# Kernel optimization log

Measured on AMD Instinct MI355X. Metric: run time of the kernel, lower is better.

Reference implementation:

```python
import math
import jax, jax.numpy as jnp
import numpy as np

NUM_HEADS = 16

def _alibi_slopes(n):
    def pow2(n):
        start = 2 ** (-2 ** (-(math.log2(n) - 3)))
        return [start * start ** i for i in range(n)]
    if math.log2(n).is_integer():
        return pow2(n)
    c = 2 ** math.floor(math.log2(n))
    return pow2(c) + _alibi_slopes(2 * c)[0::2][: n - c]

def _alibi_bias(num_heads, L):
    pos = np.arange(L)
    rel = (pos[None, :] - pos[:, None]).astype(np.float32)  # [L, L]
    slopes = np.asarray(_alibi_slopes(num_heads), dtype=np.float32)[:, None, None]
    bias = slopes * rel[None, :, :]  # [H, L, L]
    causal = pos[None, :] <= pos[:, None]
    bias = np.where(causal[None, :, :], bias, -np.inf).astype(np.float32)
    return jnp.asarray(bias)[None]  # [1, H, L, L]

def setup_inputs() -> dict:
    key = jax.random.key(0)
    ks = jax.random.split(key, 4)
    B, L, D = 2, 2048, 1024
    x = jax.random.normal(ks[0], (B, L, D), dtype=jnp.float32)
    W_in = jax.random.normal(ks[1], (D, 3 * D), dtype=jnp.float32) * 0.02
    b_in = jnp.zeros((3 * D,), dtype=jnp.float32)
    W_out = jax.random.normal(ks[2], (D, D), dtype=jnp.float32) * 0.02
    b_out = jnp.zeros((D,), dtype=jnp.float32)
    return {"x": x, "W_in": W_in, "b_in": b_in, "W_out": W_out, "b_out": b_out}

def reference(x, W_in, b_in, W_out, b_out):
    B, L, D = x.shape
    H = NUM_HEADS
    Dh = D // H
    qkv = x @ W_in + b_in  # [B, L, 3D]
    q, k, v = jnp.split(qkv, 3, axis=-1)
    # [B, H, L, Dh]
    q = q.reshape(B, L, H, Dh).transpose(0, 2, 1, 3)
    k = k.reshape(B, L, H, Dh).transpose(0, 2, 1, 3)
    v = v.reshape(B, L, H, Dh).transpose(0, 2, 1, 3)
    attn = jnp.einsum("bhqd,bhkd->bhqk", q, k) * (1.0 / math.sqrt(Dh))
    attn = attn + _alibi_bias(H, L)  # ALiBi + causal mask (-inf above diag)
    p = jax.nn.softmax(attn, axis=-1)
    out = jnp.einsum("bhqk,bhkd->bhqd", p, v)
    out = out.transpose(0, 2, 1, 3).reshape(B, L, D)
    out = out @ W_out + b_out
    return out, k, v
```

## Files before the change

### kernel.cpp

```cpp
#include <hip/hip_runtime.h>
#include <math.h>

typedef __bf16 bf16x8 __attribute__((ext_vector_type(8)));
typedef float  f32x4  __attribute__((ext_vector_type(4)));
typedef unsigned short u16x4 __attribute__((ext_vector_type(4)));

#define BATCH  2
#define SEQ    2048
#define DMODEL 1024
#define NHEAD  16
#define DHEAD  64
#define MROWS  4096
#define N_QKV  3072
#define KDIM   1024
#define OUTSECT (MROWS*DMODEL)

__device__ inline __bf16 f2bf(float f) {
    unsigned u = __builtin_bit_cast(unsigned, f);
    unsigned r = (u + 0x7fffu + ((u >> 16) & 1u)) >> 16;
    return __builtin_bit_cast(__bf16, (unsigned short)r);
}

__device__ inline void gload16(const void* g, void* l) {
    __builtin_amdgcn_global_load_lds(
        (const __attribute__((address_space(1))) void*)g,
        (__attribute__((address_space(3))) void*)l, 16, 0, 0);
}


__global__ __launch_bounds__(256) void cvt_x_k(const float* __restrict__ x,
                                               __bf16* __restrict__ xb) {
    size_t i = (size_t)blockIdx.x * 256 + threadIdx.x;
    const float4* p = (const float4*)x + i * 2;
    float4 a = p[0], b = p[1];
    __bf16 o[8] = {f2bf(a.x), f2bf(a.y), f2bf(a.z), f2bf(a.w),
                   f2bf(b.x), f2bf(b.y), f2bf(b.z), f2bf(b.w)};
    *(bf16x8*)(xb + i * 8) = *(bf16x8*)o;
}

__global__ __launch_bounds__(256) void cvt_wt_k(const float* __restrict__ W,
                                                __bf16* __restrict__ Wt, int Nw) {
    __shared__ float t[64][65];
    const int k0 = blockIdx.y * 64, n0 = blockIdx.x * 64;
    const int tid = threadIdx.x;
    #pragma unroll
    for (int u = 0; u < 4; ++u) {
        int idx = u * 256 + tid;
        int r = idx >> 4, c4 = (idx & 15) << 2;
        float4 v = *(const float4*)&W[(size_t)(k0 + r) * Nw + n0 + c4];
        t[r][c4] = v.x; t[r][c4 + 1] = v.y; t[r][c4 + 2] = v.z; t[r][c4 + 3] = v.w;
    }
    __syncthreads();
    #pragma unroll
    for (int u = 0; u < 2; ++u) {
        int idx = u * 256 + tid;
        int n = idx >> 3, k8 = (idx & 7) << 3;
        __bf16 o[8];
        #pragma unroll
        for (int i = 0; i < 8; ++i) o[i] = f2bf(t[k8 + i][n]);
        *(bf16x8*)&Wt[(size_t)(n0 + n) * KDIM + k0 + k8] = *(bf16x8*)o;
    }
}

template<int MODE, int FI, int FJ>
__global__ __launch_bounds__(256) void gemm_bf(
    const __bf16* __restrict__ A, const __bf16* __restrict__ Bt,
    const float* __restrict__ bias,
    float* __restrict__ fo, float* __restrict__ kf, float* __restrict__ vf,
    __bf16* __restrict__ qb, __bf16* __restrict__ kb, __bf16* __restrict__ vb,
    int nbx)
{
    constexpr int BMt = FI * 32, BNt = FJ * 32;
    __shared__ __align__(16) __bf16 As[BMt * 64];
    __shared__ __align__(16) __bf16 Bs[BNt * 64];

    const int tid = threadIdx.x, wid = tid >> 6, lane = tid & 63;
    const int l16 = lane & 15, lq = lane >> 4;
    const int wm = wid >> 1, wn = wid & 1;

    const int nwg = gridDim.x;
    const int bid = blockIdx.x;
    const int swz = (bid & 7) * (nwg >> 3) + (bid >> 3);
    const int m0 = (swz / nbx) * BMt;
    const int n0 = (swz % nbx) * BNt;

    const int lr8 = lane >> 3;
    const int colE = ((lane & 7) ^ lr8) << 3;

    f32x4 acc[FI][FJ];
    #pragma unroll
    for (int i = 0; i < FI; ++i)
        #pragma unroll
        for (int j = 0; j < FJ; ++j)
            acc[i][j] = f32x4{0.f, 0.f, 0.f, 0.f};

    for (int k0 = 0; k0 < KDIM; k0 += 64) {
        __syncthreads();
        #pragma unroll
        for (int c = wid; c < FI * 4 + FJ * 4; c += 4) {
            const bool isA = (c < FI * 4);
            const int ch = isA ? c : c - FI * 4;
            const int row = ch * 8 + lr8;
            const __bf16* src = isA ? (A  + (size_t)(m0 + row) * KDIM + k0 + colE)
                                    : (Bt + (size_t)(n0 + row) * KDIM + k0 + colE);
            gload16(src, (isA ? As : Bs) + ch * 512);
        }
        __syncthreads();
        #pragma unroll
        for (int kk = 0; kk < 2; ++kk) {
            bf16x8 af[FI], bfg[FJ];
            #pragma unroll
            for (int i = 0; i < FI; ++i) {
                int r = wm * (FI * 16) + i * 16 + l16;
                af[i] = *(const bf16x8*)&As[r * 64 + ((kk * 32 + lq * 8) ^ ((r & 7) << 3))];
            }
            #pragma unroll
            for (int j = 0; j < FJ; ++j) {
                int r = wn * (FJ * 16) + j * 16 + l16;
                bfg[j] = *(const bf16x8*)&Bs[r * 64 + ((kk * 32 + lq * 8) ^ ((r & 7) << 3))];
            }
            #pragma unroll
            for (int i = 0; i < FI; ++i)
                #pragma unroll
                for (int j = 0; j < FJ; ++j)
                    acc[i][j] = __builtin_amdgcn_mfma_f32_16x16x32_bf16(af[i], bfg[j], acc[i][j], 0, 0, 0);
        }
    }

    #pragma unroll
    for (int i = 0; i < FI; ++i) {
        #pragma unroll
        for (int j = 0; j < FJ; ++j) {
            const int col  = n0 + wn * (FJ * 16) + j * 16 + l16;
            const int rowb = m0 + wm * (FI * 16) + i * 16 + lq * 4;
            float v[4];
            #pragma unroll
            for (int r = 0; r < 4; ++r) v[r] = acc[i][j][r] + bias[col];
            if (MODE == 1) {
                #pragma unroll
                for (int r = 0; r < 4; ++r)
                    fo[(size_t)(rowb + r) * DMODEL + col] = v[r];
            } else {
                const int which = col >> 10, rem = col & 1023;
                const int h = rem >> 6, dh = rem & 63;
                const int bb = rowb >> 11, ll = rowb & 2047;
                const size_t lidx = ((size_t)(bb * NHEAD + h) * SEQ + ll) * DHEAD + dh;
                if (which == 0) {
                    #pragma unroll
                    for (int r = 0; r < 4; ++r) qb[lidx + (size_t)r * DHEAD] = f2bf(v[r]);
                } else if (which == 1) {
                    #pragma unroll
                    for (int r = 0; r < 4; ++r) {
                        kf[lidx + (size_t)r * DHEAD] = v[r];
                        kb[lidx + (size_t)r * DHEAD] = f2bf(v[r]);
                    }
                } else {
                    u16x4 pk;
                    #pragma unroll
                    for (int r = 0; r < 4; ++r) {
                        vf[lidx + (size_t)r * DHEAD] = v[r];
                        pk[r] = __builtin_bit_cast(unsigned short, f2bf(v[r]));
                    }
                    *(u16x4*)&vb[((size_t)(bb * NHEAD + h) * DHEAD + dh) * SEQ + ll] = pk;
                }
            }
        }
    }
}

__global__ __launch_bounds__(256) void attn_k(
    const __bf16* __restrict__ Qb, const __bf16* __restrict__ Kb,
    const __bf16* __restrict__ Vb, __bf16* __restrict__ Ob)
{
    __shared__ __align__(16) __bf16 Qs[64 * 64];
    __shared__ __align__(16) __bf16 Ks[2][64 * 64];
    __shared__ __align__(16) __bf16 Vs[2][64 * 64];
    __shared__ __align__(16) __bf16 Ps[4 * 16 * 64];

    const int tid = threadIdx.x, wid = tid >> 6, lane = tid & 63;
    const int l16 = lane & 15, lq = lane >> 4;

    const int bid = blockIdx.x;
    const int t   = bid >> 3;
    const int qt  = 31 - (t >> 2);
    const int bh  = (bid & 7) * 4 + (t & 3);
    const int h = bh & 15, bb = bh >> 4;
    const int q0 = qt * 64;
    const size_t kvbase = (size_t)bh * SEQ * DHEAD;
    const float slope = exp2f(-0.5f * (float)(h + 1));
    const int qr0 = wid * 16;
    const int lr8 = lane >> 3;
    const int colE = ((lane & 7) ^ lr8) << 3;

    #pragma unroll
    for (int u = 0; u < 2; ++u) {
        int ch = u * 4 + wid;
        int row = ch * 8 + lr8;
        gload16(Qb + kvbase + (size_t)(q0 + row) * DHEAD + colE, Qs + ch * 512);
    }
    #pragma unroll
    for (int u = 0; u < 2; ++u) {
        int ch = u * 4 + wid;
        int row = ch * 8 + lr8;
        gload16(Kb + kvbase + (size_t)row * DHEAD + colE, Ks[0] + ch * 512);
        gload16(Vb + kvbase + (size_t)row * SEQ  + colE, Vs[0] + ch * 512);
    }
    __syncthreads();

    float mrow[4], lrow[4];
    f32x4 accO[4];
    #pragma unroll
    for (int r = 0; r < 4; ++r) { mrow[r] = -1e30f; lrow[r] = 0.f; }
    #pragma unroll
    for (int j = 0; j < 4; ++j) accO[j] = f32x4{0.f, 0.f, 0.f, 0.f};

    int cur = 0;
    for (int jt = 0; jt <= qt; ++jt) {
        const int j0 = jt * 64;

        if (jt < qt) {
            const int jn = j0 + 64;
            #pragma unroll
            for (int u = 0; u < 2; ++u) {
                int ch = u * 4 + wid;
                int row = ch * 8 + lr8;
                gload16(Kb + kvbase + (size_t)(jn + row) * DHEAD + colE, Ks[cur ^ 1] + ch * 512);
                gload16(Vb + kvbase + (size_t)row * SEQ + jn + colE,     Vs[cur ^ 1] + ch * 512);
            }
        }

        f32x4 s[4];
        #pragma unroll
        for (int nf = 0; nf < 4; ++nf) s[nf] = f32x4{0.f, 0.f, 0.f, 0.f};
        const int qrow = qr0 + l16;
        bf16x8 aq0 = *(const bf16x8*)&Qs[qrow * 64 + ((lq * 8) ^ ((qrow & 7) << 3))];
        bf16x8 aq1 = *(const bf16x8*)&Qs[qrow * 64 + ((32 + lq * 8) ^ ((qrow & 7) << 3))];
        __builtin_amdgcn_s_setprio(1);
        #pragma unroll
        for (int nf = 0; nf < 4; ++nf) {
            int kr = nf * 16 + l16;
            bf16x8 bk0 = *(const bf16x8*)&Ks[cur][kr * 64 + ((lq * 8) ^ ((kr & 7) << 3))];
            bf16x8 bk1 = *(const bf16x8*)&Ks[cur][kr * 64 + ((32 + lq * 8) ^ ((kr & 7) << 3))];
            s[nf] = __builtin_amdgcn_mfma_f32_16x16x32_bf16(aq0, bk0, s[nf], 0, 0, 0);
            s[nf] = __builtin_amdgcn_mfma_f32_16x16x32_bf16(aq1, bk1, s[nf], 0, 0, 0);
        }
        __builtin_amdgcn_s_setprio(0);

        #pragma unroll
        for (int r = 0; r < 4; ++r) {
            const int qi = q0 + qr0 + lq * 4 + r;
            float rm = -1e30f;
            #pragma unroll
            for (int nf = 0; nf < 4; ++nf) {
                int ki = j0 + nf * 16 + l16;
                float sc = s[nf][r] * 0.125f;
                sc = (ki <= qi) ? (sc + slope * (float)(ki - qi)) : -1e30f;
                s[nf][r] = sc;
                rm = fmaxf(rm, sc);
            }
            #pragma unroll
            for (int msk = 1; msk < 16; msk <<= 1)
                rm = fmaxf(rm, __shfl_xor(rm, msk));
            float mnew = fmaxf(mrow[r], rm);
            float rsum = 0.f;
            const int prow = lq * 4 + r;
            #pragma unroll
            for (int nf = 0; nf < 4; ++nf) {
                float p = __expf(s[nf][r] - mnew);
                Ps[wid * 1024 + prow * 64 + ((nf * 16 + l16) ^ ((prow & 7) << 3))] = f2bf(p);
                rsum += p;
            }
            #pragma unroll
            for (int msk = 1; msk < 16; msk <<= 1)
                rsum += __shfl_xor(rsum, msk);
            float scale = __expf(mrow[r] - mnew);
            lrow[r] = lrow[r] * scale + rsum;
            mrow[r] = mnew;
            #pragma unroll
            for (int nf = 0; nf < 4; ++nf) accO[nf][r] *= scale;
        }

        bf16x8 ap0 = *(const bf16x8*)&Ps[wid * 1024 + l16 * 64 + ((lq * 8) ^ ((l16 & 7) << 3))];
        bf16x8 ap1 = *(const bf16x8*)&Ps[wid * 1024 + l16 * 64 + ((32 + lq * 8) ^ ((l16 & 7) << 3))];
        __builtin_amdgcn_s_setprio(1);
        #pragma unroll
        for (int nf = 0; nf < 4; ++nf) {
            int vr = nf * 16 + l16;
            bf16x8 bv0 = *(const bf16x8*)&Vs[cur][vr * 64 + ((lq * 8) ^ ((vr & 7) << 3))];
            bf16x8 bv1 = *(const bf16x8*)&Vs[cur][vr * 64 + ((32 + lq * 8) ^ ((vr & 7) << 3))];
            accO[nf] = __builtin_amdgcn_mfma_f32_16x16x32_bf16(ap0, bv0, accO[nf], 0, 0, 0);
            accO[nf] = __builtin_amdgcn_mfma_f32_16x16x32_bf16(ap1, bv1, accO[nf], 0, 0, 0);
        }
        __builtin_amdgcn_s_setprio(0);

        __syncthreads();
        cur ^= 1;
    }

    #pragma unroll
    for (int nf = 0; nf < 4; ++nf) {
        #pragma unroll
        for (int r = 0; r < 4; ++r) {
            int qi = q0 + qr0 + lq * 4 + r;
            int dh = nf * 16 + l16;
            Ob[(size_t)(bb * SEQ + qi) * DMODEL + h * DHEAD + dh] = f2bf(accO[nf][r] / lrow[r]);
        }
    }
}

extern "C" void kernel_launch(void* const* d_in, const int* in_sizes, int n_in,
                              void* d_out, int out_size, void* d_ws, size_t ws_size,
                              hipStream_t stream) {
    const float* x     = (const float*)d_in[0];
    const float* W_in  = (const float*)d_in[1];
    const float* b_in  = (const float*)d_in[2];
    const float* W_out = (const float*)d_in[3];
    const float* b_out = (const float*)d_in[4];

    float* out = (float*)d_out;
    float* kf  = out + (size_t)OUTSECT;
    float* vf  = out + 2 * (size_t)OUTSECT;

    __bf16* qb = (__bf16*)d_out;
    __bf16* xb = (__bf16*)d_out + (size_t)OUTSECT;

    __bf16* ob  = (__bf16*)d_ws;
    __bf16* kb  = ob + (size_t)OUTSECT;
    __bf16* vb  = kb + (size_t)OUTSECT;
    __bf16* wti = vb + (size_t)OUTSECT;
    __bf16* wto = wti + (size_t)N_QKV * KDIM;

    cvt_x_k <<<2048, 256, 0, stream>>>(x, xb);
    cvt_wt_k<<<dim3(48, 16), 256, 0, stream>>>(W_in,  wti, N_QKV);
    cvt_wt_k<<<dim3(16, 16), 256, 0, stream>>>(W_out, wto, DMODEL);

    gemm_bf<0, 4, 4><<<768, 256, 0, stream>>>(xb, wti, b_in,
        nullptr, kf, vf, qb, kb, vb, N_QKV / 128);

    attn_k<<<1024, 256, 0, stream>>>(qb, kb, vb, ob);

    gemm_bf<1, 2, 4><<<512, 256, 0, stream>>>(ob, wto, b_out,
        out, nullptr, nullptr, nullptr, nullptr, nullptr, DMODEL / 128);
}
```

Measured before the change: 222.6 us.

## Fold softmax scale into Q, seed scores with ALiBi bias, use DPP reductions

Q is pre-scaled by 1/sqrt(d)*log2e in the QKV GEMM epilogue, so the attention loop uses exp2 directly. Score accumulators are initialised with an incrementally updated ALiBi bias, and the causal mask applies only on the diagonal tile, which removes per-element scaling, bias and compare work. Row max and sum reductions use DPP instead of shuffles, and the final normalisation multiplies by a reciprocal. The trade-off is that bias accumulation through repeated float adds may drift slightly, and the changes to bf16 rounding and bias ordering alter numerics a little.

```diff
diff --git a/kernel.cpp b/kernel.cpp
--- a/kernel.cpp
+++ b/kernel.cpp
@@ -15,6 +15,9 @@
 #define KDIM   1024
 #define OUTSECT (MROWS*DMODEL)
 
+#define LOG2E 1.44269504088896f
+#define QSCALE (0.125f * LOG2E)
+
 __device__ inline __bf16 f2bf(float f) {
     unsigned u = __builtin_bit_cast(unsigned, f);
     unsigned r = (u + 0x7fffu + ((u >> 16) & 1u)) >> 16;
@@ -25,6 +28,39 @@
     __builtin_amdgcn_global_load_lds(
         (const __attribute__((address_space(1))) void*)g,
         (__attribute__((address_space(3))) void*)l, 16, 0, 0);
+}
+
+__device__ inline float dpp_max16(float x) {
+    int v, t;
+    v = __builtin_bit_cast(int, x);
+    t = __builtin_amdgcn_update_dpp(v, v, 0xB1, 0xF, 0xF, false);
+    x = fmaxf(x, __builtin_bit_cast(float, t));
+    v = __builtin_bit_cast(int, x);
+    t = __builtin_amdgcn_update_dpp(v, v, 0x4E, 0xF, 0xF, false);
+    x = fmaxf(x, __builtin_bit_cast(float, t));
+    v = __builtin_bit_cast(int, x);
+    t = __builtin_amdgcn_update_dpp(v, v, 0x128, 0xF, 0xF, false);
+    x = fmaxf(x, __builtin_bit_cast(float, t));
+    v = __builtin_bit_cast(int, x);
+    t = __builtin_amdgcn_update_dpp(v, v, 0x140, 0xF, 0xF, false);
+    x = fmaxf(x, __builtin_bit_cast(float, t));
+    return x;
+}
+__device__ inline float dpp_sum16(float x) {
+    int v, t;
+    v = __builtin_bit_cast(int, x);
+    t = __builtin_amdgcn_update_dpp(v, v, 0xB1, 0xF, 0xF, false);
+    x += __builtin_bit_cast(float, t);
+    v = __builtin_bit_cast(int, x);
+    t = __builtin_amdgcn_update_dpp(v, v, 0x4E, 0xF, 0xF, false);
+    x += __builtin_bit_cast(float, t);
+    v = __builtin_bit_cast(int, x);
+    t = __builtin_amdgcn_update_dpp(v, v, 0x128, 0xF, 0xF, false);
+    x += __builtin_bit_cast(float, t);
+    v = __builtin_bit_cast(int, x);
+    t = __builtin_amdgcn_update_dpp(v, v, 0x140, 0xF, 0xF, false);
+    x += __builtin_bit_cast(float, t);
+    return x;
 }
 
 
@@ -147,7 +183,8 @@
                 const size_t lidx = ((size_t)(bb * NHEAD + h) * SEQ + ll) * DHEAD + dh;
                 if (which == 0) {
                     #pragma unroll
-                    for (int r = 0; r < 4; ++r) qb[lidx + (size_t)r * DHEAD] = f2bf(v[r]);
+                    for (int r = 0; r < 4; ++r)
+                        qb[lidx + (size_t)r * DHEAD] = f2bf(v[r] * QSCALE);
                 } else if (which == 1) {
                     #pragma unroll
                     for (int r = 0; r < 4; ++r) {
@@ -187,7 +224,7 @@
     const int h = bh & 15, bb = bh >> 4;
     const int q0 = qt * 64;
     const size_t kvbase = (size_t)bh * SEQ * DHEAD;
-    const float slope = exp2f(-0.5f * (float)(h + 1));
+    const float slope2 = exp2f(-0.5f * (float)(h + 1)) * LOG2E;
     const int qr0 = wid * 16;
     const int lr8 = lane >> 3;
     const int colE = ((lane & 7) ^ lr8) << 3;
@@ -207,6 +244,16 @@
     }
     __syncthreads();
 
+    float ct[4][4];
+    #pragma unroll
+    for (int r = 0; r < 4; ++r) {
+        const int qi = q0 + qr0 + lq * 4 + r;
+        #pragma unroll
+        for (int nf = 0; nf < 4; ++nf)
+            ct[r][nf] = slope2 * (float)(nf * 16 + l16 - qi);
+    }
+    const float dtj = slope2 * 64.f;
+
     float mrow[4], lrow[4];
     f32x4 accO[4];
     #pragma unroll
@@ -216,10 +263,8 @@
 
     int cur = 0;
     for (int jt = 0; jt <= qt; ++jt) {
-        const int j0 = jt * 64;
-
         if (jt < qt) {
-            const int jn = j0 + 64;
+            const int jn = (jt + 1) * 64;
             #pragma unroll
             for (int u = 0; u < 2; ++u) {
                 int ch = u * 4 + wid;
@@ -231,7 +276,18 @@
 
         f32x4 s[4];
         #pragma unroll
-        for (int nf = 0; nf < 4; ++nf) s[nf] = f32x4{0.f, 0.f, 0.f, 0.f};
+        for (int nf = 0; nf < 4; ++nf) {
+            #pragma unroll
+            for (int r = 0; r < 4; ++r) s[nf][r] = ct[r][nf];
+        }
+        if (jt == qt) {
+            #pragma unroll
+            for (int nf = 0; nf < 4; ++nf)
+                #pragma unroll
+                for (int r = 0; r < 4; ++r)
+                    if (nf * 16 + l16 > qr0 + lq * 4 + r) s[nf][r] = -3e38f;
+        }
+
         const int qrow = qr0 + l16;
         bf16x8 aq0 = *(const bf16x8*)&Qs[qrow * 64 + ((lq * 8) ^ ((qrow & 7) << 3))];
         bf16x8 aq1 = *(const bf16x8*)&Qs[qrow * 64 + ((32 + lq * 8) ^ ((qrow & 7) << 3))];
@@ -248,37 +304,31 @@
 
         #pragma unroll
         for (int r = 0; r < 4; ++r) {
-            const int qi = q0 + qr0 + lq * 4 + r;
-            float rm = -1e30f;
-            #pragma unroll
-            for (int nf = 0; nf < 4; ++nf) {
-                int ki = j0 + nf * 16 + l16;
-                float sc = s[nf][r] * 0.125f;
-                sc = (ki <= qi) ? (sc + slope * (float)(ki - qi)) : -1e30f;
-                s[nf][r] = sc;
-                rm = fmaxf(rm, sc);
-            }
-            #pragma unroll
-            for (int msk = 1; msk < 16; msk <<= 1)
-                rm = fmaxf(rm, __shfl_xor(rm, msk));
+            float rm = fmaxf(fmaxf(s[0][r], s[1][r]), fmaxf(s[2][r], s[3][r]));
+            rm = dpp_max16(rm);
             float mnew = fmaxf(mrow[r], rm);
-            float rsum = 0.f;
+            float p0 = __builtin_amdgcn_exp2f(s[0][r] - mnew);
+            float p1 = __builtin_amdgcn_exp2f(s[1][r] - mnew);
+            float p2 = __builtin_amdgcn_exp2f(s[2][r] - mnew);
+            float p3 = __builtin_amdgcn_exp2f(s[3][r] - mnew);
             const int prow = lq * 4 + r;
-            #pragma unroll
-            for (int nf = 0; nf < 4; ++nf) {
-                float p = __expf(s[nf][r] - mnew);
-                Ps[wid * 1024 + prow * 64 + ((nf * 16 + l16) ^ ((prow & 7) << 3))] = f2bf(p);
-                rsum += p;
-            }
-            #pragma unroll
-            for (int msk = 1; msk < 16; msk <<= 1)
-                rsum += __shfl_xor(rsum, msk);
-            float scale = __expf(mrow[r] - mnew);
+            const int pb = wid * 1024 + prow * 64;
+            const int px = (prow & 7) << 3;
+            Ps[pb + ((l16     ) ^ px)] = (__bf16)p0;
+            Ps[pb + ((l16 + 16) ^ px)] = (__bf16)p1;
+            Ps[pb + ((l16 + 32) ^ px)] = (__bf16)p2;
+            Ps[pb + ((l16 + 48) ^ px)] = (__bf16)p3;
+            float rsum = dpp_sum16((p0 + p1) + (p2 + p3));
+            float scale = __builtin_amdgcn_exp2f(mrow[r] - mnew);
             lrow[r] = lrow[r] * scale + rsum;
             mrow[r] = mnew;
             #pragma unroll
             for (int nf = 0; nf < 4; ++nf) accO[nf][r] *= scale;
         }
+        #pragma unroll
+        for (int r = 0; r < 4; ++r)
+            #pragma unroll
+            for (int nf = 0; nf < 4; ++nf) ct[r][nf] += dtj;
 
         bf16x8 ap0 = *(const bf16x8*)&Ps[wid * 1024 + l16 * 64 + ((lq * 8) ^ ((l16 & 7) << 3))];
         bf16x8 ap1 = *(const bf16x8*)&Ps[wid * 1024 + l16 * 64 + ((32 + lq * 8) ^ ((l16 & 7) << 3))];
@@ -298,12 +348,13 @@
     }
 
     #pragma unroll
-    for (int nf = 0; nf < 4; ++nf) {
-        #pragma unroll
-        for (int r = 0; r < 4; ++r) {
-            int qi = q0 + qr0 + lq * 4 + r;
+    for (int r = 0; r < 4; ++r) {
+        const float inv = __builtin_amdgcn_rcpf(lrow[r]);
+        const int qi = q0 + qr0 + lq * 4 + r;
+        #pragma unroll
+        for (int nf = 0; nf < 4; ++nf) {
             int dh = nf * 16 + l16;
-            Ob[(size_t)(bb * SEQ + qi) * DMODEL + h * DHEAD + dh] = f2bf(accO[nf][r] / lrow[r]);
+            Ob[(size_t)(bb * SEQ + qi) * DMODEL + h * DHEAD + dh] = (__bf16)(accO[nf][r] * inv);
         }
     }
 }
```

Result: faster. 203.9 us (-8.4%).
